# Kernel optimization log

Measured on AMD Instinct MI355X. Metric: run time of the kernel, lower is better.

## Reference

```python
import jax, jax.numpy as jnp
import numpy as np

EPS = 1e-5
BS, NA, NC, NL, NPTS, ED, NG = 1, 900, 6, 4, 13, 256, 8
GD = ED // NG
IMG_W, IMG_H = 704.0, 256.0
FMAP_HW = [(64, 176), (32, 88), (16, 44), (8, 22)]


def _ln(x, g, b):
    m = x.mean(-1, keepdims=True)
    v = ((x - m) ** 2).mean(-1, keepdims=True)
    return (x - m) / jnp.sqrt(v + EPS) * g + b


def _grid_sample(img, grid):
    # img: [N,C,H,W]; grid: [N,P,Q,2] in [-1,1]; bilinear, zeros padding, align_corners=False
    N, C, H, W = img.shape
    gx = jnp.clip((grid[..., 0] + 1.0) * (W * 0.5) - 0.5, -1e4, 1e4)
    gy = jnp.clip((grid[..., 1] + 1.0) * (H * 0.5) - 0.5, -1e4, 1e4)
    x0 = jnp.floor(gx); y0 = jnp.floor(gy)
    wx1 = gx - x0; wy1 = gy - y0; wx0 = 1.0 - wx1; wy0 = 1.0 - wy1
    x0i = x0.astype(jnp.int32); y0i = y0.astype(jnp.int32)
    flat = img.reshape(N, C, H * W)

    def corner(xi, yi, wgt):
        valid = (xi >= 0) & (xi < W) & (yi >= 0) & (yi < H)
        idx = (jnp.clip(yi, 0, H - 1) * W + jnp.clip(xi, 0, W - 1))
        g = jax.vmap(lambda f, i: f[:, i])(flat, idx.reshape(N, -1))  # [N,C,P*Q]
        g = g.reshape(N, C, idx.shape[1], idx.shape[2])
        return g * (wgt * valid)[:, None]

    return (corner(x0i, y0i, wx0 * wy0) + corner(x0i + 1, y0i, wx1 * wy0)
            + corner(x0i, y0i + 1, wx0 * wy1) + corner(x0i + 1, y0i + 1, wx1 * wy1))


def setup_inputs() -> dict:
    key = jax.random.key(0)
    ks = jax.random.split(key, 20)
    d = {}
    d['instance_feature'] = jax.random.normal(ks[0], (BS, NA, ED), jnp.float32)
    xyz = jax.random.normal(ks[1], (BS, NA, 3), jnp.float32) * 1.5
    size = jax.random.normal(ks[2], (BS, NA, 3), jnp.float32) * 0.3
    theta = jax.random.uniform(ks[3], (BS, NA, 1), jnp.float32) * (2.0 * np.pi)
    vel = jax.random.normal(ks[4], (BS, NA, 3), jnp.float32) * 0.1
    d['anchor'] = jnp.concatenate([xyz, size, jnp.sin(theta), jnp.cos(theta), vel], -1)
    d['anchor_embed'] = jax.random.normal(ks[5], (BS, NA, ED), jnp.float32)
    for i, (h, w) in enumerate(FMAP_HW):
        d[f'fmap{i}'] = jax.random.normal(ks[6 + i], (BS, NC, ED, h, w), jnp.float32)
    base = jnp.array([[80., 0., 0., 352.], [0., 80., 0., 128.],
                      [0., 0., 0., 1.], [0., 0., 0., 1.]], jnp.float32)
    proj = jnp.tile(base, (BS, NC, 1, 1))
    proj = proj.at[:, :, :2, :].add(jax.random.normal(ks[10], (BS, NC, 2, 4), jnp.float32) * 2.0)
    d['projection_mat'] = proj
    d['image_wh'] = jnp.broadcast_to(jnp.array([IMG_W, IMG_H], jnp.float32), (BS, NC, 2))
    d['fix_scale'] = jnp.array([[0, 0, 0], [0.45, 0, 0], [-0.45, 0, 0], [0, 0.45, 0],
                                [0, -0.45, 0], [0, 0, 0.45], [0, 0, -0.45]], jnp.float32)

    def w(k, shape):
        return jax.random.normal(k, shape, jnp.float32) * 0.02

    d['lfc_w'] = w(ks[11], (ED, 6 * 3)); d['lfc_b'] = jnp.zeros((18,), jnp.float32)
    d['cam_w1'] = w(ks[12], (12, ED)); d['cam_b1'] = jnp.zeros((ED,), jnp.float32)
    d['cam_g1'] = jnp.ones((ED,), jnp.float32); d['cam_be1'] = jnp.zeros((ED,), jnp.float32)
    d['cam_w2'] = w(ks[13], (ED, ED)); d['cam_b2'] = jnp.zeros((ED,), jnp.float32)
    d['cam_g2'] = jnp.ones((ED,), jnp.float32); d['cam_be2'] = jnp.zeros((ED,), jnp.float32)
    d['wfc_w'] = w(ks[14], (ED, NG * NL * NPTS)); d['wfc_b'] = jnp.zeros((NG * NL * NPTS,), jnp.float32)
    d['op_w'] = w(ks[15], (ED, ED)); d['op_b'] = jnp.zeros((ED,), jnp.float32)
    return d


def reference(instance_feature, anchor, anchor_embed, fmap0, fmap1, fmap2, fmap3,
              projection_mat, image_wh, fix_scale, lfc_w, lfc_b,
              cam_w1, cam_b1, cam_g1, cam_be1, cam_w2, cam_b2, cam_g2, cam_be2,
              wfc_w, wfc_b, op_w, op_b):
    bs, na = instance_feature.shape[:2]
    # ---- keypoint generation ----
    size = jnp.exp(anchor[..., None, 3:6])                       # [bs,na,1,3]
    kp = fix_scale * size                                        # [bs,na,7,3]
    ls = jax.nn.sigmoid(instance_feature @ lfc_w + lfc_b).reshape(bs, na, -1, 3) - 0.5
    kp = jnp.concatenate([kp, ls * size], axis=-2)               # [bs,na,NPTS,3]
    sin, cos = anchor[..., 6:7], anchor[..., 7:8]                # [bs,na,1]
    kx, ky, kz = kp[..., 0], kp[..., 1], kp[..., 2]
    key_points = jnp.stack([cos * kx - sin * ky, sin * kx + cos * ky, kz], -1) \
                 + anchor[..., None, 0:3]                        # [bs,na,NPTS,3]
    # ---- per-cam/level/point group weights ----
    feat = instance_feature + anchor_embed
    cam_in = projection_mat[:, :, :3].reshape(bs, NC, 12)
    h = jax.nn.relu(cam_in @ cam_w1 + cam_b1); h = _ln(h, cam_g1, cam_be1)
    h = jax.nn.relu(h @ cam_w2 + cam_b2); cam_embed = _ln(h, cam_g2, cam_be2)
    f = feat[:, :, None] + cam_embed[:, None]                    # [bs,na,NC,ED]
    wts = (f @ wfc_w + wfc_b).reshape(bs, na, NC * NL * NPTS, NG)
    wts = jax.nn.softmax(wts, axis=-2).reshape(bs, na, NC, NL, NPTS, NG)
    # ---- multi-cam projection + bilinear sampling ----
    pts = jnp.concatenate([key_points, jnp.ones_like(key_points[..., :1])], -1)
    p2d = jnp.einsum('bcij,banj->bcani', projection_mat, pts)    # [bs,NC,na,NPTS,4]
    p2d = p2d[..., :2] / jnp.maximum(p2d[..., 2:3], 1e-5)
    p2d = p2d / image_wh[:, :, None, None]
    grid = (p2d * 2.0 - 1.0).reshape(bs * NC, na, NPTS, 2)
    feats = jnp.stack([_grid_sample(fm.reshape(bs * NC, ED, fm.shape[-2], fm.shape[-1]), grid)
                       for fm in (fmap0, fmap1, fmap2, fmap3)], axis=1)  # [bs*NC,NL,ED,na,NPTS]
    feats = feats.reshape(bs, NC, NL, ED, na, NPTS).transpose(0, 4, 1, 2, 5, 3)  # [bs,na,NC,NL,NPTS,ED]
    # ---- group-weighted fusion over cams & levels, then sum over points ----
    fg = feats.reshape(bs, na, NC, NL, NPTS, NG, GD)
    fused = jnp.einsum('bnclpg,bnclpgd->bnpgd', wts, fg).reshape(bs, na, NPTS, ED)
    fused = fused.sum(axis=2)                                    # [bs,na,ED]
    out = fused @ op_w + op_b
    return jnp.concatenate([out, instance_feature], axis=-1)     # [bs,na,2*ED]
```

## Files before the change

### kernel.cpp

```cpp
#include <hip/hip_runtime.h>
#include <stdint.h>

#define NA 900
#define NC 6
#define NL 4
#define NPTS 13
#define ED 256
#define NG 8
#define LNEPS 1e-5f
#define NSTAGE 718303
#define NSTAGE_BLOCKS 2806
#define NSAMP 312

struct PIn { const void* p[24]; };

__device__ __forceinline__ float b2f(unsigned short u){
  union { uint32_t i; float f; } v; v.i = ((uint32_t)u)<<16; return v.f;
}
__device__ __forceinline__ unsigned short f2b(float f){
  union { float f; uint32_t i; } v; v.f = f;
  uint32_t r = v.i + 0x7FFFu + ((v.i>>16)&1u);
  return (unsigned short)(r>>16);
}
#define BLO(u) __uint_as_float((u)<<16)
#define BHI(u) __uint_as_float((u)&0xffff0000u)

__device__ __forceinline__ bool sniff_bf(const unsigned short* __restrict__ u16){
  int lane = threadIdx.x & 63;
  unsigned short u = u16[2*lane];
  int e = (u>>7)&0xFF;
  int sane = (e>=110 && e<=135) ? 1 : 0;
  #pragma unroll
  for (int m=32;m;m>>=1) sane += __shfl_xor(sane, m);
  return sane >= 48;
}

__device__ __forceinline__ void blockReduce2(float& a, float& b, float* lds){
  #pragma unroll
  for (int m=32;m;m>>=1){ a += __shfl_xor(a,m); b += __shfl_xor(b,m); }
  int w = threadIdx.x>>6;
  if ((threadIdx.x&63)==0){ lds[w]=a; lds[w+4]=b; }
  __syncthreads();
  a = lds[0]+lds[1]+lds[2]+lds[3];
  b = lds[4]+lds[5]+lds[6]+lds[7];
  __syncthreads();
}

__global__ __launch_bounds__(256) void k_megaA(PIn in, float* __restrict__ stage,
                                               unsigned short* __restrict__ tf){
  const bool bf = sniff_bf((const unsigned short*)in.p[0]);
  const int b = blockIdx.x, tid = threadIdx.x;
  if (b < NSTAGE_BLOCKS){
    const int cum[21] = {0,230400,240300,470700,470796,470808,470829,475437,475455,
                         478527,478783,479039,479295,544831,545087,545343,545599,
                         652095,652511,718047,718303};
    const int map[20] = {0,1,2,7,8,9,10,11,12,13,14,15,16,17,18,19,20,21,22,23};
    int idx = b*256 + tid;
    if (idx >= NSTAGE) return;
    int seg = 0, base = 0;
    #pragma unroll
    for (int s=1;s<20;s++) if (idx >= cum[s]){ seg = s; base = cum[s]; }
    const void* src = in.p[map[0]];
    #pragma unroll
    for (int s=1;s<20;s++) if (seg==s) src = in.p[map[s]];
    int off = idx - base;
    stage[idx] = bf ? b2f(((const unsigned short*)src)[off]) : ((const float*)src)[off];
    return;
  }
  int bt = b - NSTAGE_BLOCKS;
  int l, local;
  if      (bt < 4224){ l=0; local=bt;      }
  else if (bt < 5280){ l=1; local=bt-4224; }
  else if (bt < 5544){ l=2; local=bt-5280; }
  else               { l=3; local=bt-5544; }
  const int xb[4]  = {176,44,11,3};
  const int HWs[4] = {11264,2816,704,176};
  const int TFO[4] = {0,17301504,21626880,22708224};
  int pt = local % xb[l]; int rest = local / xb[l];
  int ct = rest & 3; int c = rest >> 2;
  const void* src = in.p[3+l];
  unsigned short* dst = tf + TFO[l];
  const int HW = HWs[l];
  __shared__ unsigned short t[64][65];
  const size_t sbase = (size_t)(c*ED + ct*64)*HW + pt*64;
  #pragma unroll
  for (int i=0;i<16;i++){
    int idx = tid + i*256; int r = idx>>6, q = idx&63;
    int px = pt*64+q;
    unsigned short v = 0;
    if (px < HW){
      size_t a = sbase + (size_t)r*HW + q;
      v = bf ? ((const unsigned short*)src)[a] : f2b(((const float*)src)[a]);
    }
    t[q][r] = v;
  }
  __syncthreads();
  unsigned short* d = dst + (size_t)c*HW*ED + ct*64;
  #pragma unroll
  for (int i=0;i<16;i++){
    int idx = tid + i*256; int p = idx>>6, ch = idx&63;
    int px = pt*64+p;
    if (px < HW) d[(size_t)px*ED + ch] = t[p][ch];
  }
}

__global__ __launch_bounds__(256) void k_megaB(
    const float* __restrict__ s_proj,
    const float* __restrict__ s_w1, const float* __restrict__ s_b1,
    const float* __restrict__ s_g1, const float* __restrict__ s_be1,
    const float* __restrict__ s_w2, const float* __restrict__ s_b2,
    const float* __restrict__ s_g2, const float* __restrict__ s_be2,
    const float* __restrict__ s_wfcw, const float* __restrict__ s_wfcb,
    const float* __restrict__ s_inst, const float* __restrict__ s_anc,
    const float* __restrict__ s_fixs, const float* __restrict__ s_lw,
    const float* __restrict__ s_lb, const float* __restrict__ s_imwh,
    float* __restrict__ Bc, float* __restrict__ pxpy){
  const int b = blockIdx.x, tid = threadIdx.x;
  if (b < 42){
    const int c = b/7, colt = b - (b/7)*7;
    __shared__ float h[ED];
    __shared__ float cE[ED];
    __shared__ float red[8];
    __shared__ float part[4][64];
    float ci[12];
    #pragma unroll
    for (int i=0;i<12;i++) ci[i] = s_proj[c*16+i];
    float acc = s_b1[tid];
    #pragma unroll
    for (int k=0;k<12;k++) acc += ci[k]*s_w1[k*ED+tid];
    float x = fmaxf(acc, 0.f);
    float s=x, q=x*x;
    blockReduce2(s,q,red);
    float mean = s*(1.f/ED), var = q*(1.f/ED)-mean*mean;
    h[tid] = (x-mean)*rsqrtf(var+LNEPS)*s_g1[tid] + s_be1[tid];
    __syncthreads();
    acc = s_b2[tid];
    #pragma unroll 8
    for (int k=0;k<ED;k++) acc += h[k]*s_w2[k*ED+tid];
    x = fmaxf(acc,0.f);
    s=x; q=x*x;
    blockReduce2(s,q,red);
    mean = s*(1.f/ED); var = q*(1.f/ED)-mean*mean;
    cE[tid] = (x-mean)*rsqrtf(var+LNEPS)*s_g2[tid] + s_be2[tid];
    __syncthreads();
    const int kc = tid>>6, colL = tid&63, col = colt*64+colL;
    float a = 0.f;
    if (col < 416){
      #pragma unroll 8
      for (int k=0;k<64;k++) a += cE[kc*64+k]*s_wfcw[(kc*64+k)*416+col];
    }
    part[kc][colL] = a;
    __syncthreads();
    if (kc==0 && col<416)
      Bc[c*416+col] = part[0][colL]+part[1][colL]+part[2][colL]+part[3][colL] + s_wfcb[col];
    return;
  }
  const int n = b - 42;
  __shared__ float ifs[ED];
  __shared__ float ls[18];
  __shared__ float kp[13][3];
  __shared__ float sc[8];
  ifs[tid] = s_inst[n*ED+tid];
  if (tid < 3)       sc[tid] = s_anc[n*11+tid];
  else if (tid == 3) sc[3]   = s_anc[n*11+6];
  else if (tid == 4) sc[4]   = s_anc[n*11+7];
  else if (tid < 8)  sc[tid] = __expf(s_anc[n*11+tid-2]);
  __syncthreads();
  if (tid < 18){
    float a = s_lb[tid];
    for (int k=0;k<ED;k++) a += ifs[k]*s_lw[k*18+tid];
    ls[tid] = 1.f/(1.f+__expf(-a)) - 0.5f;
  }
  __syncthreads();
  if (tid < 13){
    float kx,ky,kz;
    if (tid < 7){
      kx = s_fixs[tid*3+0]*sc[5];
      ky = s_fixs[tid*3+1]*sc[6];
      kz = s_fixs[tid*3+2]*sc[7];
    } else {
      int j = tid-7;
      kx = ls[j*3+0]*sc[5]; ky = ls[j*3+1]*sc[6]; kz = ls[j*3+2]*sc[7];
    }
    kp[tid][0] = sc[4]*kx - sc[3]*ky + sc[0];
    kp[tid][1] = sc[3]*kx + sc[4]*ky + sc[1];
    kp[tid][2] = kz + sc[2];
  }
  __syncthreads();
  if (tid < NC*NPTS){
    int c = tid/NPTS, p = tid - c*NPTS;
    float m[12];
    #pragma unroll
    for (int i=0;i<12;i++) m[i] = s_proj[c*16+i];
    float X=kp[p][0], Y=kp[p][1], Z=kp[p][2];
    float x = m[0]*X + m[1]*Y + m[2]*Z  + m[3];
    float y = m[4]*X + m[5]*Y + m[6]*Z  + m[7];
    float z = m[8]*X + m[9]*Y + m[10]*Z + m[11];
    float d = fmaxf(z, 1e-5f);
    float iw = s_imwh[c*2+0], ih = s_imwh[c*2+1];
    int o = ((n*NC+c)*NPTS+p)*2;
    pxpy[o]   = x/(d*iw);
    pxpy[o+1] = y/(d*ih);
  }
}

__global__ __launch_bounds__(256) void k_megaC(
    const float* __restrict__ s_inst, const float* __restrict__ s_ae,
    const float* __restrict__ s_wfcw, const float* __restrict__ Bc,
    const float* __restrict__ pxpy,
    float* __restrict__ logits, uint4* __restrict__ desc){
  const int b = blockIdx.x, tid = threadIdx.x;
  if (b < 1575){
    const int cg = b % 7, ag = b / 7;
    const int tx = tid&63, ty = tid>>6;
    const int col = cg*64 + tx;
    const int a   = ag*4 + ty;
    __shared__ float fs[4][ED];
    #pragma unroll
    for (int i=0;i<4;i++){
      int an = ag*4 + i;
      float v = 0.f;
      if (an < NA) v = s_inst[an*ED+tid] + s_ae[an*ED+tid];
      fs[i][tid] = v;
    }
    __syncthreads();
    if (col >= 416 || a >= NA) return;
    float acc = 0.f;
    #pragma unroll 8
    for (int k=0;k<ED;k++) acc += fs[ty][k]*s_wfcw[k*416+col];
    #pragma unroll
    for (int c=0;c<NC;c++)
      logits[(a*NC+c)*416 + col] = acc + Bc[c*416+col];
    return;
  }
  int t = (b-1575)*256 + tid;
  if (t >= NA*NSAMP) return;
  int n = t/NSAMP, s = t - n*NSAMP;
  int c = s/52, rr = s - c*52;
  int l = rr/13, p = rr - l*13;
  int o = ((n*NC+c)*NPTS+p)*2;
  float px = pxpy[o], py = pxpy[o+1];
  const int W = 176>>l, H = 64>>l;
  const int TFO[4] = {0,17301504,21626880,22708224};
  float gx = fminf(fmaxf(px*(float)W - 0.5f, -10000.f), 10000.f);
  float gy = fminf(fmaxf(py*(float)H - 0.5f, -10000.f), 10000.f);
  float xf = floorf(gx), yf = floorf(gy);
  int x0 = (int)xf, y0 = (int)yf;
  float wx1 = gx-xf, wy1 = gy-yf;
  float wx0 = 1.f-wx1, wy0 = 1.f-wy1;
  bool vx0 = (x0>=0)&&(x0<W),   vx1 = (x0+1>=0)&&(x0+1<W);
  bool vy0 = (y0>=0)&&(y0<H),   vy1 = (y0+1>=0)&&(y0+1<H);
  float w00 = (vx0&&vy0) ? wx0*wy0 : 0.f;
  float w10 = (vx1&&vy0) ? wx1*wy0 : 0.f;
  float w01 = (vx0&&vy1) ? wx0*wy1 : 0.f;
  float w11 = (vx1&&vy1) ? wx1*wy1 : 0.f;
  int cx0 = min(max(x0,0),W-1), cx1 = min(max(x0+1,0),W-1);
  int cy0 = min(max(y0,0),H-1), cy1 = min(max(y0+1,0),H-1);
  uint32_t cam = (uint32_t)TFO[l] + (uint32_t)c*H*W*ED;
  uint4 bi;
  bi.x = cam + (uint32_t)(cy0*W+cx0)*ED;
  bi.y = cam + (uint32_t)(cy0*W+cx1)*ED;
  bi.z = cam + (uint32_t)(cy1*W+cx0)*ED;
  bi.w = cam + (uint32_t)(cy1*W+cx1)*ED;
  uint4 wv;
  wv.x = __float_as_uint(w00); wv.y = __float_as_uint(w10);
  wv.z = __float_as_uint(w01); wv.w = __float_as_uint(w11);
  desc[t*2]   = bi;
  desc[t*2+1] = wv;
}

__global__ __launch_bounds__(256) void k_sample(
    const unsigned short* __restrict__ tf, const uint4* __restrict__ desc,
    const float* __restrict__ logits, float* __restrict__ fused){
  const int n = blockIdx.x, half = blockIdx.y, tid = threadIdx.x;
  __shared__ float wl[NSAMP*NG];
  __shared__ float red[8][ED];
  {
    const int g = tid>>5, j = tid&31;
    float v[10]; float m = -1e30f;
    #pragma unroll
    for (int i=0;i<10;i++){
      int e = j + 32*i;
      float val = -1e30f;
      if (e < NSAMP){
        int c = e/52, rr = e - c*52;
        val = logits[(n*NC+c)*416 + rr*8 + g];
        m = fmaxf(m, val);
      }
      v[i] = val;
    }
    #pragma unroll
    for (int mk=16;mk;mk>>=1) m = fmaxf(m, __shfl_xor(m, mk, 32));
    float sum = 0.f;
    #pragma unroll
    for (int i=0;i<10;i++){
      if (j + 32*i < NSAMP){ float ex = __expf(v[i]-m); v[i] = ex; sum += ex; }
    }
    #pragma unroll
    for (int mk=16;mk;mk>>=1) sum += __shfl_xor(sum, mk, 32);
    float inv = 1.f/sum;
    #pragma unroll
    for (int i=0;i<10;i++){
      int e = j + 32*i;
      if (e < NSAMP) wl[e*8+g] = v[i]*inv;
    }
  }
  __syncthreads();
  const int grp = tid>>6, lane = tid&63;
  const int sub = lane>>5, lane32 = lane&31;
  const int ch8 = lane32*8, gg = lane32>>2;
  const int strm = grp*2 + sub;
  float acc[8] = {0,0,0,0,0,0,0,0};
  const int sBeg = half*156;
  for (int i=0;i<20;i++){
    int s = i*8 + strm;
    if (s >= 156) break;
    int t = n*NSAMP + sBeg + s;
    uint4 bi = desc[t*2];
    uint4 wf = desc[t*2+1];
    float w00 = __uint_as_float(wf.x), w10 = __uint_as_float(wf.y);
    float w01 = __uint_as_float(wf.z), w11 = __uint_as_float(wf.w);
    if (w00+w10+w01+w11 == 0.f) continue;
    float wg = wl[(sBeg+s)*8+gg];
    uint4 q00 = *reinterpret_cast<const uint4*>(tf + bi.x + ch8);
    uint4 q10 = *reinterpret_cast<const uint4*>(tf + bi.y + ch8);
    uint4 q01 = *reinterpret_cast<const uint4*>(tf + bi.z + ch8);
    uint4 q11 = *reinterpret_cast<const uint4*>(tf + bi.w + ch8);
    acc[0] += wg*(w00*BLO(q00.x)+w10*BLO(q10.x)+w01*BLO(q01.x)+w11*BLO(q11.x));
    acc[1] += wg*(w00*BHI(q00.x)+w10*BHI(q10.x)+w01*BHI(q01.x)+w11*BHI(q11.x));
    acc[2] += wg*(w00*BLO(q00.y)+w10*BLO(q10.y)+w01*BLO(q01.y)+w11*BLO(q11.y));
    acc[3] += wg*(w00*BHI(q00.y)+w10*BHI(q10.y)+w01*BHI(q01.y)+w11*BHI(q11.y));
    acc[4] += wg*(w00*BLO(q00.z)+w10*BLO(q10.z)+w01*BLO(q01.z)+w11*BLO(q11.z));
    acc[5] += wg*(w00*BHI(q00.z)+w10*BHI(q10.z)+w01*BHI(q01.z)+w11*BHI(q11.z));
    acc[6] += wg*(w00*BLO(q00.w)+w10*BLO(q10.w)+w01*BLO(q01.w)+w11*BLO(q11.w));
    acc[7] += wg*(w00*BHI(q00.w)+w10*BHI(q10.w)+w01*BHI(q01.w)+w11*BHI(q11.w));
  }
  *reinterpret_cast<float4*>(&red[strm][ch8])   = make_float4(acc[0],acc[1],acc[2],acc[3]);
  *reinterpret_cast<float4*>(&red[strm][ch8+4]) = make_float4(acc[4],acc[5],acc[6],acc[7]);
  __syncthreads();
  float r = 0.f;
  #pragma unroll
  for (int i=0;i<8;i++) r += red[i][tid];
  fused[(half*NA + n)*ED + tid] = r;
}

__global__ __launch_bounds__(256) void k_out(
    const float* __restrict__ fused, const float* __restrict__ opw,
    const float* __restrict__ opb, const float* __restrict__ inst,
    const void* __restrict__ rawinst, void* __restrict__ outv){
  const int tid = threadIdx.x;
  const int a0 = blockIdx.x*8;
  const bool bf = sniff_bf((const unsigned short*)rawinst);
  __shared__ float fs[8][ED];
  #pragma unroll
  for (int i=0;i<8;i++){
    int a = a0+i;
    fs[i][tid] = (a<NA) ? (fused[a*ED+tid] + fused[(NA+a)*ED+tid]) : 0.f;
  }
  __syncthreads();
  float bias = opb[tid];
  float acc[8];
  #pragma unroll
  for (int i=0;i<8;i++) acc[i]=bias;
  #pragma unroll 4
  for (int k=0;k<ED;k++){
    float wv = opw[k*ED+tid];
    #pragma unroll
    for (int i=0;i<8;i++) acc[i] += fs[i][k]*wv;
  }
  #pragma unroll
  for (int i=0;i<8;i++){
    int a = a0+i;
    if (a<NA){
      float pv = inst[a*ED+tid];
      if (bf){
        unsigned short* outh = (unsigned short*)outv;
        outh[a*512+tid]     = f2b(acc[i]);
        outh[a*512+256+tid] = f2b(pv);
      } else {
        float* outf = (float*)outv;
        outf[a*512+tid]     = acc[i];
        outf[a*512+256+tid] = pv;
      }
    }
  }
}

extern "C" void kernel_launch(void* const* d_in, const int* in_sizes, int n_in,
                              void* d_out, int out_size, void* d_ws, size_t ws_size,
                              hipStream_t stream){
  char* ws = (char*)d_ws;
  size_t off = 0;
  auto alloc = [&](size_t bytes)->char*{
    char* p = ws + off; off += (bytes + 63) & ~size_t(63); return p;
  };
  unsigned short* tf = (unsigned short*)alloc((size_t)22978560*2);
  float* stage  = (float*)alloc((size_t)NSTAGE*4);
  float* Bc     = (float*)alloc((size_t)NC*416*4);
  float* pxpy   = (float*)alloc((size_t)NA*NC*NPTS*2*4);
  float* logits = (float*)alloc((size_t)NA*NC*416*4);
  uint4* desc   = (uint4*)alloc((size_t)NA*NSAMP*32);
  float* fused  = (float*)alloc((size_t)2*NA*ED*4);

  float* s_inst = stage + 0;
  float* s_anc  = stage + 230400;
  float* s_ae   = stage + 240300;
  float* s_proj = stage + 470700;
  float* s_imwh = stage + 470796;
  float* s_fixs = stage + 470808;
  float* s_lw   = stage + 470829;
  float* s_lb   = stage + 475437;
  float* s_w1   = stage + 475455;
  float* s_b1   = stage + 478527;
  float* s_g1   = stage + 478783;
  float* s_be1  = stage + 479039;
  float* s_w2   = stage + 479295;
  float* s_b2   = stage + 544831;
  float* s_g2   = stage + 545087;
  float* s_be2  = stage + 545343;
  float* s_wfcw = stage + 545599;
  float* s_wfcb = stage + 652095;
  float* s_opw  = stage + 652511;
  float* s_opb  = stage + 718047;

  PIn in;
  for (int i=0;i<24;i++) in.p[i] = d_in[i];

  k_megaA<<<NSTAGE_BLOCKS + 5616, 256, 0, stream>>>(in, stage, tf);
  k_megaB<<<42 + NA, 256, 0, stream>>>(s_proj, s_w1,s_b1,s_g1,s_be1, s_w2,s_b2,s_g2,s_be2,
                                       s_wfcw, s_wfcb, s_inst, s_anc, s_fixs, s_lw, s_lb,
                                       s_imwh, Bc, pxpy);
  k_megaC<<<1575 + 1097, 256, 0, stream>>>(s_inst, s_ae, s_wfcw, Bc, pxpy, logits, desc);
  k_sample<<<dim3(NA,2), 256, 0, stream>>>(tf, desc, logits, fused);
  k_out<<<(NA+7)/8, 256, 0, stream>>>(fused, s_opw, s_opb, s_inst, d_in[0], d_out);
}
```

Measured before the change: 297.3 us.

## Fuse five-kernel pipeline into prep and per-anchor fused kernel

Collapses the five launches into two. The prep kernel does staging, a vectorized fmap transpose to bf16, and the camera-embedding MLP, which now reads the raw inputs directly. A single per-anchor kernel then computes the keypoints, the logits/softmax in LDS, the sample descriptors, the bilinear gathers and the output projection. This removes the global round-trips for pxpy, logits, descriptors and fused, and cuts launch count. The cost is large per-block LDS (logits plus descriptors plus the reduction buffer), only 900 blocks with one anchor each instead of split halves, and per-anchor reloads of the wfc and op weights with no batching across anchors.

```diff
diff --git a/kernel.cpp b/kernel.cpp
--- a/kernel.cpp
+++ b/kernel.cpp
@@ -10,6 +10,7 @@
 #define LNEPS 1e-5f
 #define NSTAGE 718303
 #define NSTAGE_BLOCKS 2806
+#define NTRANS 5616
 #define NSAMP 312
 
 struct PIn { const void* p[24]; };
@@ -24,6 +25,10 @@
 }
 #define BLO(u) __uint_as_float((u)<<16)
 #define BHI(u) __uint_as_float((u)&0xffff0000u)
+
+__device__ __forceinline__ float ldx(const void* p, int i, bool bf){
+  return bf ? b2f(((const unsigned short*)p)[i]) : ((const float*)p)[i];
+}
 
 __device__ __forceinline__ bool sniff_bf(const unsigned short* __restrict__ u16){
   int lane = threadIdx.x & 63;
@@ -46,10 +51,19 @@
   __syncthreads();
 }
 
-__global__ __launch_bounds__(256) void k_megaA(PIn in, float* __restrict__ stage,
-                                               unsigned short* __restrict__ tf){
+__global__ __launch_bounds__(256) void k_prep(PIn in, float* __restrict__ stage,
+                                              unsigned short* __restrict__ tf,
+                                              float* __restrict__ Bc){
   const bool bf = sniff_bf((const unsigned short*)in.p[0]);
-  const int b = blockIdx.x, tid = threadIdx.x;
+  const int tid = threadIdx.x;
+  int b = blockIdx.x;
+
+  __shared__ unsigned short T[64][68];
+  __shared__ float h[ED];
+  __shared__ float cE[ED];
+  __shared__ float red8[8];
+  __shared__ float part[4][64];
+
   if (b < NSTAGE_BLOCKS){
     const int cum[21] = {0,230400,240300,470700,470796,470808,470829,475437,475455,
                          478527,478783,479039,479295,544831,545087,545343,545599,
@@ -63,113 +77,161 @@
     const void* src = in.p[map[0]];
     #pragma unroll
     for (int s=1;s<20;s++) if (seg==s) src = in.p[map[s]];
-    int off = idx - base;
-    stage[idx] = bf ? b2f(((const unsigned short*)src)[off]) : ((const float*)src)[off];
+    stage[idx] = ldx(src, idx - base, bf);
     return;
   }
-  int bt = b - NSTAGE_BLOCKS;
-  int l, local;
-  if      (bt < 4224){ l=0; local=bt;      }
-  else if (bt < 5280){ l=1; local=bt-4224; }
-  else if (bt < 5544){ l=2; local=bt-5280; }
-  else               { l=3; local=bt-5544; }
-  const int xb[4]  = {176,44,11,3};
-  const int HWs[4] = {11264,2816,704,176};
-  const int TFO[4] = {0,17301504,21626880,22708224};
-  int pt = local % xb[l]; int rest = local / xb[l];
-  int ct = rest & 3; int c = rest >> 2;
-  const void* src = in.p[3+l];
-  unsigned short* dst = tf + TFO[l];
-  const int HW = HWs[l];
-  __shared__ unsigned short t[64][65];
-  const size_t sbase = (size_t)(c*ED + ct*64)*HW + pt*64;
-  #pragma unroll
-  for (int i=0;i<16;i++){
-    int idx = tid + i*256; int r = idx>>6, q = idx&63;
-    int px = pt*64+q;
-    unsigned short v = 0;
-    if (px < HW){
-      size_t a = sbase + (size_t)r*HW + q;
-      v = bf ? ((const unsigned short*)src)[a] : f2b(((const float*)src)[a]);
-    }
-    t[q][r] = v;
-  }
-  __syncthreads();
-  unsigned short* d = dst + (size_t)c*HW*ED + ct*64;
-  #pragma unroll
-  for (int i=0;i<16;i++){
-    int idx = tid + i*256; int p = idx>>6, ch = idx&63;
-    int px = pt*64+p;
-    if (px < HW) d[(size_t)px*ED + ch] = t[p][ch];
-  }
-}
-
-__global__ __launch_bounds__(256) void k_megaB(
-    const float* __restrict__ s_proj,
-    const float* __restrict__ s_w1, const float* __restrict__ s_b1,
-    const float* __restrict__ s_g1, const float* __restrict__ s_be1,
-    const float* __restrict__ s_w2, const float* __restrict__ s_b2,
-    const float* __restrict__ s_g2, const float* __restrict__ s_be2,
-    const float* __restrict__ s_wfcw, const float* __restrict__ s_wfcb,
-    const float* __restrict__ s_inst, const float* __restrict__ s_anc,
-    const float* __restrict__ s_fixs, const float* __restrict__ s_lw,
-    const float* __restrict__ s_lb, const float* __restrict__ s_imwh,
-    float* __restrict__ Bc, float* __restrict__ pxpy){
-  const int b = blockIdx.x, tid = threadIdx.x;
-  if (b < 42){
+  b -= NSTAGE_BLOCKS;
+  if (b < NTRANS){
+    const int xb[4]  = {176,44,11,3};
+    const int HWs[4] = {11264,2816,704,176};
+    const int TFO[4] = {0,17301504,21626880,22708224};
+    int l, local;
+    if      (b < 4224){ l=0; local=b;      }
+    else if (b < 5280){ l=1; local=b-4224; }
+    else if (b < 5544){ l=2; local=b-5280; }
+    else              { l=3; local=b-5544; }
+    int pt = local % xb[l]; int rest = local / xb[l];
+    int ct = rest & 3; int c = rest >> 2;
+    const int HW = HWs[l];
+    const int px0 = pt*64;
+    const void* src = in.p[3+l];
+    #pragma unroll
+    for (int p=0;p<2;p++){
+      int lch = p*32 + (tid>>3);
+      int gch = ct*64 + lch;
+      int pxv = (tid&7)*8;
+      size_t base = (size_t)(c*ED+gch)*HW + px0 + pxv;
+      unsigned short v[8];
+      if (px0 + pxv + 8 <= HW){
+        if (bf){
+          uint4 q = *reinterpret_cast<const uint4*>((const unsigned short*)src + base);
+          v[0]=q.x&0xffff; v[1]=q.x>>16; v[2]=q.y&0xffff; v[3]=q.y>>16;
+          v[4]=q.z&0xffff; v[5]=q.z>>16; v[6]=q.w&0xffff; v[7]=q.w>>16;
+        } else {
+          float4 f0 = *reinterpret_cast<const float4*>((const float*)src + base);
+          float4 f1 = *reinterpret_cast<const float4*>((const float*)src + base + 4);
+          v[0]=f2b(f0.x); v[1]=f2b(f0.y); v[2]=f2b(f0.z); v[3]=f2b(f0.w);
+          v[4]=f2b(f1.x); v[5]=f2b(f1.y); v[6]=f2b(f1.z); v[7]=f2b(f1.w);
+        }
+      } else {
+        #pragma unroll
+        for (int i=0;i<8;i++){
+          int px = px0+pxv+i;
+          v[i] = (px<HW) ? (bf ? ((const unsigned short*)src)[base+i]
+                               : f2b(((const float*)src)[base+i])) : (unsigned short)0;
+        }
+      }
+      #pragma unroll
+      for (int i=0;i<8;i++) T[pxv+i][lch] = v[i];
+    }
+    __syncthreads();
+    unsigned short* dst = tf + TFO[l] + (size_t)c*HW*ED + ct*64;
+    #pragma unroll
+    for (int p=0;p<2;p++){
+      int pxl = p*32 + (tid>>3);
+      int px = px0 + pxl;
+      if (px >= HW) continue;
+      int ch8 = (tid&7)*8;
+      ushort4 lo = *reinterpret_cast<ushort4*>(&T[pxl][ch8]);
+      ushort4 hi = *reinterpret_cast<ushort4*>(&T[pxl][ch8+4]);
+      union { ushort4 hh[2]; uint4 q; } u;
+      u.hh[0]=lo; u.hh[1]=hi;
+      *reinterpret_cast<uint4*>(dst + (size_t)px*ED + ch8) = u.q;
+    }
+    return;
+  }
+  b -= NTRANS;
+  {
+    const void* proj = in.p[7];
+    const void* w1 = in.p[12]; const void* b1 = in.p[13];
+    const void* g1 = in.p[14]; const void* be1 = in.p[15];
+    const void* w2 = in.p[16]; const void* b2 = in.p[17];
+    const void* g2 = in.p[18]; const void* be2 = in.p[19];
+    const void* wfcw = in.p[20]; const void* wfcb = in.p[21];
     const int c = b/7, colt = b - (b/7)*7;
-    __shared__ float h[ED];
-    __shared__ float cE[ED];
-    __shared__ float red[8];
-    __shared__ float part[4][64];
     float ci[12];
     #pragma unroll
-    for (int i=0;i<12;i++) ci[i] = s_proj[c*16+i];
-    float acc = s_b1[tid];
-    #pragma unroll
-    for (int k=0;k<12;k++) acc += ci[k]*s_w1[k*ED+tid];
+    for (int i=0;i<12;i++) ci[i] = ldx(proj, c*16+i, bf);
+    float acc = ldx(b1, tid, bf);
+    #pragma unroll
+    for (int k=0;k<12;k++) acc += ci[k]*ldx(w1, k*ED+tid, bf);
     float x = fmaxf(acc, 0.f);
     float s=x, q=x*x;
-    blockReduce2(s,q,red);
+    blockReduce2(s,q,red8);
     float mean = s*(1.f/ED), var = q*(1.f/ED)-mean*mean;
-    h[tid] = (x-mean)*rsqrtf(var+LNEPS)*s_g1[tid] + s_be1[tid];
+    h[tid] = (x-mean)*rsqrtf(var+LNEPS)*ldx(g1,tid,bf) + ldx(be1,tid,bf);
     __syncthreads();
-    acc = s_b2[tid];
+    acc = ldx(b2, tid, bf);
     #pragma unroll 8
-    for (int k=0;k<ED;k++) acc += h[k]*s_w2[k*ED+tid];
+    for (int k=0;k<ED;k++) acc += h[k]*ldx(w2, k*ED+tid, bf);
     x = fmaxf(acc,0.f);
     s=x; q=x*x;
-    blockReduce2(s,q,red);
+    blockReduce2(s,q,red8);
     mean = s*(1.f/ED); var = q*(1.f/ED)-mean*mean;
-    cE[tid] = (x-mean)*rsqrtf(var+LNEPS)*s_g2[tid] + s_be2[tid];
+    cE[tid] = (x-mean)*rsqrtf(var+LNEPS)*ldx(g2,tid,bf) + ldx(be2,tid,bf);
     __syncthreads();
     const int kc = tid>>6, colL = tid&63, col = colt*64+colL;
     float a = 0.f;
     if (col < 416){
       #pragma unroll 8
-      for (int k=0;k<64;k++) a += cE[kc*64+k]*s_wfcw[(kc*64+k)*416+col];
+      for (int k=0;k<64;k++) a += cE[kc*64+k]*ldx(wfcw, (kc*64+k)*416+col, bf);
     }
     part[kc][colL] = a;
     __syncthreads();
     if (kc==0 && col<416)
-      Bc[c*416+col] = part[0][colL]+part[1][colL]+part[2][colL]+part[3][colL] + s_wfcb[col];
-    return;
-  }
-  const int n = b - 42;
+      Bc[c*416+col] = part[0][colL]+part[1][colL]+part[2][colL]+part[3][colL] + ldx(wfcb,col,bf);
+  }
+}
+
+__global__ __launch_bounds__(256) void k_anchor(
+    const float* __restrict__ stage, const unsigned short* __restrict__ tf,
+    const float* __restrict__ Bc, const void* __restrict__ rawinst,
+    void* __restrict__ outv){
+  const int n = blockIdx.x, tid = threadIdx.x;
+  const bool bf = sniff_bf((const unsigned short*)rawinst);
+
+  const float* s_inst = stage + 0;
+  const float* s_anc  = stage + 230400;
+  const float* s_ae   = stage + 240300;
+  const float* s_proj = stage + 470700;
+  const float* s_imwh = stage + 470796;
+  const float* s_fixs = stage + 470808;
+  const float* s_lw   = stage + 470829;
+  const float* s_lb   = stage + 475437;
+  const float* s_wfcw = stage + 545599;
+  const float* s_opw  = stage + 652511;
+  const float* s_opb  = stage + 718047;
+
   __shared__ float ifs[ED];
-  __shared__ float ls[18];
+  __shared__ float fe[ED];
+  __shared__ float lg[NC*416];
+  __shared__ uint4 dsc[NSAMP*2];
+  __shared__ float red[8][ED];
+  __shared__ float fu[ED];
   __shared__ float kp[13][3];
   __shared__ float sc[8];
-  ifs[tid] = s_inst[n*ED+tid];
-  if (tid < 3)       sc[tid] = s_anc[n*11+tid];
-  else if (tid == 3) sc[3]   = s_anc[n*11+6];
-  else if (tid == 4) sc[4]   = s_anc[n*11+7];
-  else if (tid < 8)  sc[tid] = __expf(s_anc[n*11+tid-2]);
-  __syncthreads();
-  if (tid < 18){
-    float a = s_lb[tid];
-    for (int k=0;k<ED;k++) a += ifs[k]*s_lw[k*18+tid];
-    ls[tid] = 1.f/(1.f+__expf(-a)) - 0.5f;
+  __shared__ float lsv[18];
+
+  {
+    float iv = s_inst[n*ED+tid];
+    ifs[tid] = iv;
+    fe[tid]  = iv + s_ae[n*ED+tid];
+    if (tid < 3)       sc[tid] = s_anc[n*11+tid];
+    else if (tid == 3) sc[3]   = s_anc[n*11+6];
+    else if (tid == 4) sc[4]   = s_anc[n*11+7];
+    else if (tid < 8)  sc[tid] = __expf(s_anc[n*11+tid-2]);
+  }
+  __syncthreads();
+  if (tid < 144){
+    int d = tid>>3, j = tid&7;
+    float a = 0.f;
+    #pragma unroll 8
+    for (int k=j*32;k<j*32+32;k++) a += ifs[k]*s_lw[k*18+d];
+    a += __shfl_xor(a,1); a += __shfl_xor(a,2); a += __shfl_xor(a,4);
+    if (j==0){
+      a += s_lb[d];
+      lsv[d] = 1.f/(1.f+__expf(-a)) - 0.5f;
+    }
   }
   __syncthreads();
   if (tid < 13){
@@ -180,101 +242,71 @@
       kz = s_fixs[tid*3+2]*sc[7];
     } else {
       int j = tid-7;
-      kx = ls[j*3+0]*sc[5]; ky = ls[j*3+1]*sc[6]; kz = ls[j*3+2]*sc[7];
+      kx = lsv[j*3+0]*sc[5]; ky = lsv[j*3+1]*sc[6]; kz = lsv[j*3+2]*sc[7];
     }
     kp[tid][0] = sc[4]*kx - sc[3]*ky + sc[0];
     kp[tid][1] = sc[3]*kx + sc[4]*ky + sc[1];
     kp[tid][2] = kz + sc[2];
   }
-  __syncthreads();
-  if (tid < NC*NPTS){
-    int c = tid/NPTS, p = tid - c*NPTS;
-    float m[12];
-    #pragma unroll
-    for (int i=0;i<12;i++) m[i] = s_proj[c*16+i];
-    float X=kp[p][0], Y=kp[p][1], Z=kp[p][2];
-    float x = m[0]*X + m[1]*Y + m[2]*Z  + m[3];
-    float y = m[4]*X + m[5]*Y + m[6]*Z  + m[7];
-    float z = m[8]*X + m[9]*Y + m[10]*Z + m[11];
-    float d = fmaxf(z, 1e-5f);
-    float iw = s_imwh[c*2+0], ih = s_imwh[c*2+1];
-    int o = ((n*NC+c)*NPTS+p)*2;
-    pxpy[o]   = x/(d*iw);
-    pxpy[o+1] = y/(d*ih);
-  }
-}
-
-__global__ __launch_bounds__(256) void k_megaC(
-    const float* __restrict__ s_inst, const float* __restrict__ s_ae,
-    const float* __restrict__ s_wfcw, const float* __restrict__ Bc,
-    const float* __restrict__ pxpy,
-    float* __restrict__ logits, uint4* __restrict__ desc){
-  const int b = blockIdx.x, tid = threadIdx.x;
-  if (b < 1575){
-    const int cg = b % 7, ag = b / 7;
-    const int tx = tid&63, ty = tid>>6;
-    const int col = cg*64 + tx;
-    const int a   = ag*4 + ty;
-    __shared__ float fs[4][ED];
-    #pragma unroll
-    for (int i=0;i<4;i++){
-      int an = ag*4 + i;
-      float v = 0.f;
-      if (an < NA) v = s_inst[an*ED+tid] + s_ae[an*ED+tid];
-      fs[i][tid] = v;
-    }
-    __syncthreads();
-    if (col >= 416 || a >= NA) return;
-    float acc = 0.f;
-    #pragma unroll 8
-    for (int k=0;k<ED;k++) acc += fs[ty][k]*s_wfcw[k*416+col];
-    #pragma unroll
-    for (int c=0;c<NC;c++)
-      logits[(a*NC+c)*416 + col] = acc + Bc[c*416+col];
-    return;
-  }
-  int t = (b-1575)*256 + tid;
-  if (t >= NA*NSAMP) return;
-  int n = t/NSAMP, s = t - n*NSAMP;
-  int c = s/52, rr = s - c*52;
-  int l = rr/13, p = rr - l*13;
-  int o = ((n*NC+c)*NPTS+p)*2;
-  float px = pxpy[o], py = pxpy[o+1];
-  const int W = 176>>l, H = 64>>l;
-  const int TFO[4] = {0,17301504,21626880,22708224};
-  float gx = fminf(fmaxf(px*(float)W - 0.5f, -10000.f), 10000.f);
-  float gy = fminf(fmaxf(py*(float)H - 0.5f, -10000.f), 10000.f);
-  float xf = floorf(gx), yf = floorf(gy);
-  int x0 = (int)xf, y0 = (int)yf;
-  float wx1 = gx-xf, wy1 = gy-yf;
-  float wx0 = 1.f-wx1, wy0 = 1.f-wy1;
-  bool vx0 = (x0>=0)&&(x0<W),   vx1 = (x0+1>=0)&&(x0+1<W);
-  bool vy0 = (y0>=0)&&(y0<H),   vy1 = (y0+1>=0)&&(y0+1<H);
-  float w00 = (vx0&&vy0) ? wx0*wy0 : 0.f;
-  float w10 = (vx1&&vy0) ? wx1*wy0 : 0.f;
-  float w01 = (vx0&&vy1) ? wx0*wy1 : 0.f;
-  float w11 = (vx1&&vy1) ? wx1*wy1 : 0.f;
-  int cx0 = min(max(x0,0),W-1), cx1 = min(max(x0+1,0),W-1);
-  int cy0 = min(max(y0,0),H-1), cy1 = min(max(y0+1,0),H-1);
-  uint32_t cam = (uint32_t)TFO[l] + (uint32_t)c*H*W*ED;
-  uint4 bi;
-  bi.x = cam + (uint32_t)(cy0*W+cx0)*ED;
-  bi.y = cam + (uint32_t)(cy0*W+cx1)*ED;
-  bi.z = cam + (uint32_t)(cy1*W+cx0)*ED;
-  bi.w = cam + (uint32_t)(cy1*W+cx1)*ED;
-  uint4 wv;
-  wv.x = __float_as_uint(w00); wv.y = __float_as_uint(w10);
-  wv.z = __float_as_uint(w01); wv.w = __float_as_uint(w11);
-  desc[t*2]   = bi;
-  desc[t*2+1] = wv;
-}
-
-__global__ __launch_bounds__(256) void k_sample(
-    const unsigned short* __restrict__ tf, const uint4* __restrict__ desc,
-    const float* __restrict__ logits, float* __restrict__ fused){
-  const int n = blockIdx.x, half = blockIdx.y, tid = threadIdx.x;
-  __shared__ float wl[NSAMP*NG];
-  __shared__ float red[8][ED];
+  {
+    int col2 = (tid < 160) ? tid+256 : 415;
+    float a0 = 0.f, a1 = 0.f;
+    #pragma unroll 4
+    for (int k=0;k<ED;k++){
+      float fv = fe[k];
+      a0 += fv*s_wfcw[k*416+tid];
+      a1 += fv*s_wfcw[k*416+col2];
+    }
+    #pragma unroll
+    for (int c=0;c<NC;c++){
+      lg[c*416+tid] = a0 + Bc[c*416+tid];
+      if (tid < 160) lg[c*416+tid+256] = a1 + Bc[c*416+tid+256];
+    }
+  }
+  __syncthreads();
+  #pragma unroll
+  for (int pass=0;pass<2;pass++){
+    int s = tid + pass*256;
+    if (s < NSAMP){
+      int c = s/52, rr = s - c*52;
+      int l = rr/13, p = rr - l*13;
+      float m[12];
+      #pragma unroll
+      for (int i=0;i<12;i++) m[i] = s_proj[c*16+i];
+      float X=kp[p][0], Y=kp[p][1], Z=kp[p][2];
+      float x = m[0]*X + m[1]*Y + m[2]*Z  + m[3];
+      float y = m[4]*X + m[5]*Y + m[6]*Z  + m[7];
+      float z = m[8]*X + m[9]*Y + m[10]*Z + m[11];
+      float d = fmaxf(z, 1e-5f);
+      float px = x/(d*s_imwh[c*2+0]), py = y/(d*s_imwh[c*2+1]);
+      const int W = 176>>l, H = 64>>l;
+      const int TFO[4] = {0,17301504,21626880,22708224};
+      float gx = fminf(fmaxf(px*(float)W - 0.5f, -10000.f), 10000.f);
+      float gy = fminf(fmaxf(py*(float)H - 0.5f, -10000.f), 10000.f);
+      float xf = floorf(gx), yf = floorf(gy);
+      int x0 = (int)xf, y0 = (int)yf;
+      float wx1 = gx-xf, wy1 = gy-yf;
+      float wx0 = 1.f-wx1, wy0 = 1.f-wy1;
+      bool vx0 = (x0>=0)&&(x0<W),   vx1 = (x0+1>=0)&&(x0+1<W);
+      bool vy0 = (y0>=0)&&(y0<H),   vy1 = (y0+1>=0)&&(y0+1<H);
+      float w00 = (vx0&&vy0) ? wx0*wy0 : 0.f;
+      float w10 = (vx1&&vy0) ? wx1*wy0 : 0.f;
+      float w01 = (vx0&&vy1) ? wx0*wy1 : 0.f;
+      float w11 = (vx1&&vy1) ? wx1*wy1 : 0.f;
+      int cx0 = min(max(x0,0),W-1), cx1 = min(max(x0+1,0),W-1);
+      int cy0 = min(max(y0,0),H-1), cy1 = min(max(y0+1,0),H-1);
+      uint32_t cam = (uint32_t)TFO[l] + (uint32_t)(c*H*W)*ED;
+      uint4 bi, wv;
+      bi.x = cam + (uint32_t)(cy0*W+cx0)*ED;
+      bi.y = cam + (uint32_t)(cy0*W+cx1)*ED;
+      bi.z = cam + (uint32_t)(cy1*W+cx0)*ED;
+      bi.w = cam + (uint32_t)(cy1*W+cx1)*ED;
+      wv.x = __float_as_uint(w00); wv.y = __float_as_uint(w10);
+      wv.z = __float_as_uint(w01); wv.w = __float_as_uint(w11);
+      dsc[s*2]   = bi;
+      dsc[s*2+1] = wv;
+    }
+  }
   {
     const int g = tid>>5, j = tid&31;
     float v[10]; float m = -1e30f;
@@ -284,7 +316,7 @@
       float val = -1e30f;
       if (e < NSAMP){
         int c = e/52, rr = e - c*52;
-        val = logits[(n*NC+c)*416 + rr*8 + g];
+        val = lg[c*416 + rr*8 + g];
         m = fmaxf(m, val);
       }
       v[i] = val;
@@ -302,86 +334,63 @@
     #pragma unroll
     for (int i=0;i<10;i++){
       int e = j + 32*i;
-      if (e < NSAMP) wl[e*8+g] = v[i]*inv;
-    }
-  }
-  __syncthreads();
-  const int grp = tid>>6, lane = tid&63;
-  const int sub = lane>>5, lane32 = lane&31;
-  const int ch8 = lane32*8, gg = lane32>>2;
-  const int strm = grp*2 + sub;
-  float acc[8] = {0,0,0,0,0,0,0,0};
-  const int sBeg = half*156;
-  for (int i=0;i<20;i++){
-    int s = i*8 + strm;
-    if (s >= 156) break;
-    int t = n*NSAMP + sBeg + s;
-    uint4 bi = desc[t*2];
-    uint4 wf = desc[t*2+1];
-    float w00 = __uint_as_float(wf.x), w10 = __uint_as_float(wf.y);
-    float w01 = __uint_as_float(wf.z), w11 = __uint_as_float(wf.w);
-    if (w00+w10+w01+w11 == 0.f) continue;
-    float wg = wl[(sBeg+s)*8+gg];
-    uint4 q00 = *reinterpret_cast<const uint4*>(tf + bi.x + ch8);
-    uint4 q10 = *reinterpret_cast<const uint4*>(tf + bi.y + ch8);
-    uint4 q01 = *reinterpret_cast<const uint4*>(tf + bi.z + ch8);
-    uint4 q11 = *reinterpret_cast<const uint4*>(tf + bi.w + ch8);
-    acc[0] += wg*(w00*BLO(q00.x)+w10*BLO(q10.x)+w01*BLO(q01.x)+w11*BLO(q11.x));
-    acc[1] += wg*(w00*BHI(q00.x)+w10*BHI(q10.x)+w01*BHI(q01.x)+w11*BHI(q11.x));
-    acc[2] += wg*(w00*BLO(q00.y)+w10*BLO(q10.y)+w01*BLO(q01.y)+w11*BLO(q11.y));
-    acc[3] += wg*(w00*BHI(q00.y)+w10*BHI(q10.y)+w01*BHI(q01.y)+w11*BHI(q11.y));
-    acc[4] += wg*(w00*BLO(q00.z)+w10*BLO(q10.z)+w01*BLO(q01.z)+w11*BLO(q11.z));
-    acc[5] += wg*(w00*BHI(q00.z)+w10*BHI(q10.z)+w01*BHI(q01.z)+w11*BHI(q11.z));
-    acc[6] += wg*(w00*BLO(q00.w)+w10*BLO(q10.w)+w01*BLO(q01.w)+w11*BLO(q11.w));
-    acc[7] += wg*(w00*BHI(q00.w)+w10*BHI(q10.w)+w01*BHI(q01.w)+w11*BHI(q11.w));
-  }
-  *reinterpret_cast<float4*>(&red[strm][ch8])   = make_float4(acc[0],acc[1],acc[2],acc[3]);
-  *reinterpret_cast<float4*>(&red[strm][ch8+4]) = make_float4(acc[4],acc[5],acc[6],acc[7]);
-  __syncthreads();
-  float r = 0.f;
-  #pragma unroll
-  for (int i=0;i<8;i++) r += red[i][tid];
-  fused[(half*NA + n)*ED + tid] = r;
-}
-
-__global__ __launch_bounds__(256) void k_out(
-    const float* __restrict__ fused, const float* __restrict__ opw,
-    const float* __restrict__ opb, const float* __restrict__ inst,
-    const void* __restrict__ rawinst, void* __restrict__ outv){
-  const int tid = threadIdx.x;
-  const int a0 = blockIdx.x*8;
-  const bool bf = sniff_bf((const unsigned short*)rawinst);
-  __shared__ float fs[8][ED];
-  #pragma unroll
-  for (int i=0;i<8;i++){
-    int a = a0+i;
-    fs[i][tid] = (a<NA) ? (fused[a*ED+tid] + fused[(NA+a)*ED+tid]) : 0.f;
-  }
-  __syncthreads();
-  float bias = opb[tid];
-  float acc[8];
-  #pragma unroll
-  for (int i=0;i<8;i++) acc[i]=bias;
-  #pragma unroll 4
-  for (int k=0;k<ED;k++){
-    float wv = opw[k*ED+tid];
-    #pragma unroll
-    for (int i=0;i<8;i++) acc[i] += fs[i][k]*wv;
-  }
-  #pragma unroll
-  for (int i=0;i<8;i++){
-    int a = a0+i;
-    if (a<NA){
-      float pv = inst[a*ED+tid];
-      if (bf){
-        unsigned short* outh = (unsigned short*)outv;
-        outh[a*512+tid]     = f2b(acc[i]);
-        outh[a*512+256+tid] = f2b(pv);
-      } else {
-        float* outf = (float*)outv;
-        outf[a*512+tid]     = acc[i];
-        outf[a*512+256+tid] = pv;
+      if (e < NSAMP){
+        int c = e/52, rr = e - c*52;
+        lg[c*416 + rr*8 + g] = v[i]*inv;
       }
+    }
+  }
+  __syncthreads();
+  {
+    const int strm = tid>>5, lane32 = tid&31;
+    const int ch8 = lane32*8, gg = lane32>>2;
+    float acc[8] = {0,0,0,0,0,0,0,0};
+    for (int it=0; it<39; it++){
+      int s = it*8 + strm;
+      uint4 bi = dsc[s*2];
+      uint4 wf = dsc[s*2+1];
+      float w00 = __uint_as_float(wf.x), w10 = __uint_as_float(wf.y);
+      float w01 = __uint_as_float(wf.z), w11 = __uint_as_float(wf.w);
+      if (w00+w10+w01+w11 == 0.f) continue;
+      int c = s/52, rr = s - c*52;
+      float wg = lg[c*416 + rr*8 + gg];
+      uint4 q00 = *reinterpret_cast<const uint4*>(tf + bi.x + ch8);
+      uint4 q10 = *reinterpret_cast<const uint4*>(tf + bi.y + ch8);
+      uint4 q01 = *reinterpret_cast<const uint4*>(tf + bi.z + ch8);
+      uint4 q11 = *reinterpret_cast<const uint4*>(tf + bi.w + ch8);
+      acc[0] += wg*(w00*BLO(q00.x)+w10*BLO(q10.x)+w01*BLO(q01.x)+w11*BLO(q11.x));
+      acc[1] += wg*(w00*BHI(q00.x)+w10*BHI(q10.x)+w01*BHI(q01.x)+w11*BHI(q11.x));
+      acc[2] += wg*(w00*BLO(q00.y)+w10*BLO(q10.y)+w01*BLO(q01.y)+w11*BLO(q11.y));
+      acc[3] += wg*(w00*BHI(q00.y)+w10*BHI(q10.y)+w01*BHI(q01.y)+w11*BHI(q11.y));
+      acc[4] += wg*(w00*BLO(q00.z)+w10*BLO(q10.z)+w01*BLO(q01.z)+w11*BLO(q11.z));
+      acc[5] += wg*(w00*BHI(q00.z)+w10*BHI(q10.z)+w01*BHI(q01.z)+w11*BHI(q11.z));
+      acc[6] += wg*(w00*BLO(q00.w)+w10*BLO(q10.w)+w01*BLO(q01.w)+w11*BLO(q11.w));
+      acc[7] += wg*(w00*BHI(q00.w)+w10*BHI(q10.w)+w01*BHI(q01.w)+w11*BHI(q11.w));
+    }
+    *reinterpret_cast<float4*>(&red[strm][ch8])   = make_float4(acc[0],acc[1],acc[2],acc[3]);
+    *reinterpret_cast<float4*>(&red[strm][ch8+4]) = make_float4(acc[4],acc[5],acc[6],acc[7]);
+  }
+  __syncthreads();
+  {
+    float r = 0.f;
+    #pragma unroll
+    for (int i=0;i<8;i++) r += red[i][tid];
+    fu[tid] = r;
+  }
+  __syncthreads();
+  {
+    float acc = s_opb[tid];
+    #pragma unroll 4
+    for (int k=0;k<ED;k++) acc += fu[k]*s_opw[k*ED+tid];
+    float pv = ifs[tid];
+    if (bf){
+      unsigned short* outh = (unsigned short*)outv;
+      outh[n*512+tid]     = f2b(acc);
+      outh[n*512+256+tid] = f2b(pv);
+    } else {
+      float* outf = (float*)outv;
+      outf[n*512+tid]     = acc;
+      outf[n*512+256+tid] = pv;
     }
   }
 }
@@ -397,40 +406,10 @@
   unsigned short* tf = (unsigned short*)alloc((size_t)22978560*2);
   float* stage  = (float*)alloc((size_t)NSTAGE*4);
   float* Bc     = (float*)alloc((size_t)NC*416*4);
-  float* pxpy   = (float*)alloc((size_t)NA*NC*NPTS*2*4);
-  float* logits = (float*)alloc((size_t)NA*NC*416*4);
-  uint4* desc   = (uint4*)alloc((size_t)NA*NSAMP*32);
-  float* fused  = (float*)alloc((size_t)2*NA*ED*4);
-
-  float* s_inst = stage + 0;
-  float* s_anc  = stage + 230400;
-  float* s_ae   = stage + 240300;
-  float* s_proj = stage + 470700;
-  float* s_imwh = stage + 470796;
-  float* s_fixs = stage + 470808;
-  float* s_lw   = stage + 470829;
-  float* s_lb   = stage + 475437;
-  float* s_w1   = stage + 475455;
-  float* s_b1   = stage + 478527;
-  float* s_g1   = stage + 478783;
-  float* s_be1  = stage + 479039;
-  float* s_w2   = stage + 479295;
-  float* s_b2   = stage + 544831;
-  float* s_g2   = stage + 545087;
-  float* s_be2  = stage + 545343;
-  float* s_wfcw = stage + 545599;
-  float* s_wfcb = stage + 652095;
-  float* s_opw  = stage + 652511;
-  float* s_opb  = stage + 718047;
 
   PIn in;
   for (int i=0;i<24;i++) in.p[i] = d_in[i];
 
-  k_megaA<<<NSTAGE_BLOCKS + 5616, 256, 0, stream>>>(in, stage, tf);
-  k_megaB<<<42 + NA, 256, 0, stream>>>(s_proj, s_w1,s_b1,s_g1,s_be1, s_w2,s_b2,s_g2,s_be2,
-                                       s_wfcw, s_wfcb, s_inst, s_anc, s_fixs, s_lw, s_lb,
-                                       s_imwh, Bc, pxpy);
-  k_megaC<<<1575 + 1097, 256, 0, stream>>>(s_inst, s_ae, s_wfcw, Bc, pxpy, logits, desc);
-  k_sample<<<dim3(NA,2), 256, 0, stream>>>(tf, desc, logits, fused);
-  k_out<<<(NA+7)/8, 256, 0, stream>>>(fused, s_opw, s_opb, s_inst, d_in[0], d_out);
-}
+  k_prep<<<NSTAGE_BLOCKS + NTRANS + 42, 256, 0, stream>>>(in, stage, tf, Bc);
+  k_anchor<<<NA, 256, 0, stream>>>(stage, tf, Bc, d_in[0], d_out);
+}
```

Measured after the change: 257.1 us. 1.16x faster.
